# Optimization experiments

Hardware: AMD Instinct MI355X
Metric: run time of the kernel (lower is better)

## Reference

```python
import jax, jax.numpy as jnp
import numpy as np

N = 50000   # nodes
E = 800000  # edges (before self-loops)
IN_C, HID, OUT_C = 10, 96, 48


def setup_inputs() -> dict:
    key = jax.random.key(0)
    ks = jax.random.split(key, 8)
    x = jax.random.normal(ks[0], (N, IN_C), dtype=jnp.float32)
    edge_index = jax.random.randint(ks[1], (2, E), 0, N, dtype=jnp.int64)
    # Glorot-ish scaled weights for the three GCN layers
    W1 = jax.random.normal(ks[2], (IN_C, HID), dtype=jnp.float32) * (1.0 / np.sqrt(IN_C))
    b1 = jnp.zeros((HID,), dtype=jnp.float32)
    W_mu = jax.random.normal(ks[3], (HID, OUT_C), dtype=jnp.float32) * (1.0 / np.sqrt(HID))
    b_mu = jnp.zeros((OUT_C,), dtype=jnp.float32)
    W_logstd = jax.random.normal(ks[4], (HID, OUT_C), dtype=jnp.float32) * (1.0 / np.sqrt(HID))
    b_logstd = jnp.zeros((OUT_C,), dtype=jnp.float32)
    return {"x": x, "edge_index": edge_index, "W1": W1, "b1": b1,
            "W_mu": W_mu, "b_mu": b_mu, "W_logstd": W_logstd, "b_logstd": b_logstd}


def _gcn_norm(edge_index, n_nodes, dtype):
    # PyG gcn_norm: add self-loops, symmetric normalization D^-1/2 A D^-1/2
    loops = jnp.arange(n_nodes, dtype=edge_index.dtype)
    ei = jnp.concatenate([edge_index, jnp.stack([loops, loops])], axis=1)
    row, col = ei[0], ei[1]
    deg = jax.ops.segment_sum(jnp.ones(ei.shape[1], dtype=dtype), col, num_segments=n_nodes)
    dis = jnp.where(deg > 0, jax.lax.rsqrt(deg), jnp.zeros_like(deg))
    norm = dis[row] * dis[col]  # [E+N]
    return row, col, norm


def _gcn_conv(h, row, col, norm, W, b, n_nodes):
    hw = h @ W                                   # dense projection [N, F_out]
    msgs = hw[row] * norm[:, None]               # gather + scale   [E+N, F_out]
    out = jax.ops.segment_sum(msgs, col, num_segments=n_nodes)  # scatter-add
    return out + b


def reference(x, edge_index, W1, b1, W_mu, b_mu, W_logstd, b_logstd):
    row, col, norm = _gcn_norm(edge_index, N, x.dtype)
    h = jax.nn.relu(_gcn_conv(x, row, col, norm, W1, b1, N))
    mu = _gcn_conv(h, row, col, norm, W_mu, b_mu, N)
    logstd = _gcn_conv(h, row, col, norm, W_logstd, b_logstd, N)
    return mu, logstd
```

## Files before the change

kernel.cpp:

```cpp
#include <hip/hip_runtime.h>
#include <hip/hip_bf16.h>

#define NND 50000
#define NED 800000
#define INC 10
#define HID 96
#define OUTC 48
#define NOUT (NND*OUTC)
#define MTILES 3125
#define NW 98
#define SPAN 512
#define EW_CAP 9216
#define PB 200
#define PBE 4000

typedef __hip_bfloat16 bf16;
typedef __attribute__((ext_vector_type(8))) short short8;
typedef __attribute__((ext_vector_type(4))) float f32x4;

#define W1F_O  0L
#define B1F_O  960L
#define BMF_O  1056L
#define BLF_O  1104L
#define DIS_O  1152L
#define XS_O   51152L
#define FLOATS_TOT 551152L

__device__ __forceinline__ float b2f(bf16 v) { return __bfloat162float(v); }
__device__ __forceinline__ float bfLo(unsigned int p) { return __uint_as_float(p << 16); }
__device__ __forceinline__ float bfHi(unsigned int p) { return __uint_as_float(p & 0xffff0000u); }
__device__ __forceinline__ unsigned short f2bu(float v) {
    return __bfloat16_as_ushort(__float2bfloat16(v));
}

__global__ __launch_bounds__(256) void k_part(const int* ei, const void* x,
                                              const void* w1, const void* b1,
                                              const void* wm, const void* bm,
                                              const void* wl, const void* bl,
                                              int* flags, float* F, unsigned short* wct,
                                              unsigned int* part, int* smat, int* cmat) {
    __shared__ int s_oddnz, s_big;
    __shared__ int counts[NW], cur[NW];
    __shared__ unsigned int buf[PBE];
    int tid = threadIdx.x;
    if (tid == 0) { s_oddnz = 0; s_big = 0; }
    for (int i = tid; i < NW; i += 256) counts[i] = 0;
    __syncthreads();
    {
        if (tid < 128) {
            if (ei[2 * tid + 1] != 0) atomicOr(&s_oddnz, 1);
        }
        const unsigned short* xs = (const unsigned short*)x;
        unsigned short u = xs[tid * 8];
        float f = __uint_as_float(((unsigned int)u) << 16);
        int big = !(fabsf(f) < 64.0f);
        unsigned short u2 = xs[tid * 8 + 5];
        float f2 = __uint_as_float(((unsigned int)u2) << 16);
        big |= !(fabsf(f2) < 64.0f);
        if (big) atomicOr(&s_big, 1);
    }
    __syncthreads();
    int iw = (s_oddnz == 0) ? 1 : 0;
    int ff = s_big ? 1 : 0;
    if (blockIdx.x == 0 && tid == 0) { flags[0] = iw; flags[1] = ff; }

    if (blockIdx.x < 41) {
        int idx = blockIdx.x * 256 + tid;
        if (idx < 10368) {
            const void* src; long off; int mode; long dst = 0;
            if      (idx < 960)  { src = w1; off = idx;        mode = 0; dst = W1F_O + idx; }
            else if (idx < 1056) { src = b1; off = idx - 960;  mode = 0; dst = B1F_O + (idx - 960); }
            else if (idx < 1104) { src = bm; off = idx - 1056; mode = 0; dst = BMF_O + (idx - 1056); }
            else if (idx < 1152) { src = bl; off = idx - 1104; mode = 0; dst = BLF_O + (idx - 1104); }
            else if (idx < 5760) { src = wm; off = idx - 1152; mode = 1; }
            else                 { src = wl; off = idx - 5760; mode = 2; }
            float v = ff ? ((const float*)src)[off] : b2f(((const bf16*)src)[off]);
            if (mode == 0) F[dst] = v;
            else if (mode == 1) wct[(off % OUTC) * (long)HID + off / OUTC] = f2bu(v);
            else                wct[(OUTC + off % OUTC) * (long)HID + off / OUTC] = f2bu(v);
        }
    }

    unsigned int wreg[16];
    int base = blockIdx.x * 1000;
    for (int it = 0; it < 4; ++it) {
        int j = it * 256 + tid;
        if (j < 1000) {
            int j4 = base + j;
            int r0, r1, r2, r3, c0, c1, c2, c3;
            if (iw) {
                const int4* pr = (const int4*)ei;
                const int4* pc = (const int4*)(ei + 2L * NED);
                int4 ra = pr[2 * j4], rb = pr[2 * j4 + 1];
                int4 ca = pc[2 * j4], cb = pc[2 * j4 + 1];
                r0 = ra.x; r1 = ra.z; r2 = rb.x; r3 = rb.z;
                c0 = ca.x; c1 = ca.z; c2 = cb.x; c3 = cb.z;
            } else {
                int4 ra = ((const int4*)ei)[j4];
                int4 ca = ((const int4*)(ei + NED))[j4];
                r0 = ra.x; r1 = ra.y; r2 = ra.z; r3 = ra.w;
                c0 = ca.x; c1 = ca.y; c2 = ca.z; c3 = ca.w;
            }
            wreg[4 * it]     = (unsigned)r0 | ((unsigned)c0 << 16);
            wreg[4 * it + 1] = (unsigned)r1 | ((unsigned)c1 << 16);
            wreg[4 * it + 2] = (unsigned)r2 | ((unsigned)c2 << 16);
            wreg[4 * it + 3] = (unsigned)r3 | ((unsigned)c3 << 16);
            atomicAdd(&counts[wreg[4 * it]     >> 25], 1);
            atomicAdd(&counts[wreg[4 * it + 1] >> 25], 1);
            atomicAdd(&counts[wreg[4 * it + 2] >> 25], 1);
            atomicAdd(&counts[wreg[4 * it + 3] >> 25], 1);
        }
    }
    __syncthreads();
    if (tid < NW) {
        int run = 0;
        for (int j = 0; j < tid; ++j) run += counts[j];
        cur[tid] = run;
        cmat[tid * PB + blockIdx.x] = counts[tid];
        smat[tid * PB + blockIdx.x] = blockIdx.x * PBE + run;
    }
    __syncthreads();
    for (int it = 0; it < 4; ++it) {
        int j = it * 256 + tid;
        if (j < 1000) {
#pragma unroll
            for (int q = 0; q < 4; ++q) {
                unsigned int w = wreg[4 * it + q];
                int pos = atomicAdd(&cur[w >> 25], 1);
                buf[pos] = w;
            }
        }
    }
    __syncthreads();
    for (int i = tid; i < PBE; i += 256) part[blockIdx.x * PBE + i] = buf[i];
}

__global__ __launch_bounds__(1024) void k_win(const unsigned int* part, const int* smat,
                                              const int* cmat, const void* x, float* F,
                                              int* cnt, int* start, unsigned short* csr) {
    __shared__ int Lrun[PB], Srun[PB];
    __shared__ int hist[SPAN], st[SPAN], cur[SPAN];
    __shared__ float dl[SPAN];
    __shared__ int s_big;
    int tid = threadIdx.x;
    int w = blockIdx.x;
    if (tid == 0) s_big = 0;
    if (tid < PB) { Lrun[tid] = cmat[w * PB + tid]; Srun[tid] = smat[w * PB + tid]; }
    if (tid < SPAN) hist[tid] = 0;
    __syncthreads();
    if (tid < 256) {
        const unsigned short* xs = (const unsigned short*)x;
        unsigned short u = xs[tid * 8];
        float f = __uint_as_float(((unsigned int)u) << 16);
        int big = !(fabsf(f) < 64.0f);
        unsigned short u2 = xs[tid * 8 + 5];
        float f2 = __uint_as_float(((unsigned int)u2) << 16);
        big |= !(fabsf(f2) < 64.0f);
        if (big) atomicOr(&s_big, 1);
    }
    unsigned int lo = (unsigned)w * SPAN;
    int wave = tid >> 6, lane = tid & 63;
    for (int rb = wave; rb < PB; rb += 16) {
        int L = Lrun[rb], S = Srun[rb];
        for (int i = lane; i < L; i += 64)
            atomicAdd(&hist[(part[S + i] >> 16) - lo], 1);
    }
    __syncthreads();
    int ff = s_big;
    if (tid < SPAN) st[tid] = hist[tid];
    __syncthreads();
    for (int off = 1; off < SPAN; off <<= 1) {
        int t = (tid < SPAN && tid >= off) ? st[tid - off] : 0;
        __syncthreads();
        if (tid < SPAN) st[tid] += t;
        __syncthreads();
    }
    if (tid < SPAN) {
        int h0 = hist[tid];
        int abs0 = w * EW_CAP + (st[tid] - h0);
        cur[tid] = abs0;
        float dis = rsqrtf((float)h0 + 1.0f);
        dl[tid] = dis;
        int g = (int)lo + tid;
        if (g < NND) {
            cnt[g] = h0; start[g] = abs0;
            F[DIS_O + g] = dis;
        }
    }
    __syncthreads();
    for (int i = tid; i < SPAN * INC; i += 1024) {
        int node = (int)lo + i / INC;
        if (node < NND) {
            long xo = (long)node * INC + (i % INC);
            float xv = ff ? ((const float*)x)[xo] : b2f(((const bf16*)x)[xo]);
            F[XS_O + xo] = dl[i / INC] * xv;
        }
    }
    int lim = (w + 1) * EW_CAP;
    for (int rb = wave; rb < PB; rb += 16) {
        int L = Lrun[rb], S = Srun[rb];
        for (int i = lane; i < L; i += 64) {
            unsigned int e = part[S + i];
            int pos = atomicAdd(&cur[(e >> 16) - lo], 1);
            if (pos < lim) csr[pos] = (unsigned short)(e & 0xffffu);
        }
    }
}

__global__ __launch_bounds__(256) void k_layer1(const int* cnt, const int* start,
                                                const unsigned short* csr, const float* F,
                                                unsigned short* h) {
    __shared__ float w1s[1056];
    for (int i = threadIdx.x; i < 1056; i += 256) w1s[i] = F[W1F_O + i];
    __syncthreads();
    int idx = blockIdx.x * 256 + threadIdx.x;
    if (idx >= NND * 4) return;
    int node = idx >> 2, sub = idx & 3;
    int s = start[node], t = s + cnt[node];
    int lim = ((node >> 9) + 1) * EW_CAP;
    if (t > lim) t = lim;
    float ax[INC];
#pragma unroll
    for (int j = 0; j < INC; ++j) ax[j] = 0.0f;
    for (int k = s + sub; k < t; k += 4) {
        int src = csr[k];
        const float2* xr = (const float2*)(F + XS_O + (long)src * INC);
#pragma unroll
        for (int j = 0; j < 5; ++j) {
            float2 v = xr[j];
            ax[2 * j]     += v.x;
            ax[2 * j + 1] += v.y;
        }
    }
    if (sub == 0) {
        const float2* xr = (const float2*)(F + XS_O + (long)node * INC);
#pragma unroll
        for (int j = 0; j < 5; ++j) {
            float2 v = xr[j];
            ax[2 * j]     += v.x;
            ax[2 * j + 1] += v.y;
        }
    }
#pragma unroll
    for (int j = 0; j < INC; ++j) {
        ax[j] += __shfl_xor(ax[j], 1, 64);
        ax[j] += __shfl_xor(ax[j], 2, 64);
    }
    float dn = F[DIS_O + node];
#pragma unroll
    for (int j = 0; j < INC; ++j) ax[j] *= dn;
    int f0 = sub * 24;
    unsigned int* hrow = (unsigned int*)(h + (size_t)node * HID);
#pragma unroll
    for (int f = f0; f < f0 + 24; f += 2) {
        float a0 = w1s[960 + f], a1 = w1s[960 + f + 1];
#pragma unroll
        for (int kk = 0; kk < INC; ++kk) {
            a0 = fmaf(ax[kk], w1s[kk * HID + f], a0);
            a1 = fmaf(ax[kk], w1s[kk * HID + f + 1], a1);
        }
        a0 = fmaxf(a0, 0.0f) * dn;
        a1 = fmaxf(a1, 0.0f) * dn;
        unsigned int u0 = f2bu(a0), u1 = f2bu(a1);
        hrow[f >> 1] = u0 | (u1 << 16);
    }
}

__global__ __launch_bounds__(256) void k_gaggh(const int* cnt, const int* start,
                                               const unsigned short* csr, const float* F,
                                               const unsigned short* h, unsigned int* v) {
    int wid = threadIdx.x >> 6;
    int lane = threadIdx.x & 63;
    int node = blockIdx.x * 4 + wid;
    if (lane >= 48) return;
    const unsigned int* hb = (const unsigned int*)h;

    int s = start[node], t = s + cnt[node];
    int lim = ((node >> 9) + 1) * EW_CAP;
    if (t > lim) t = lim;
    float a0 = 0.0f, a1 = 0.0f;
    int k = s;
    for (; k + 7 < t; k += 8) {
        int s0 = csr[k],     s1 = csr[k + 1], s2 = csr[k + 2], s3 = csr[k + 3];
        int s4 = csr[k + 4], s5 = csr[k + 5], s6 = csr[k + 6], s7 = csr[k + 7];
        unsigned int p0 = hb[(size_t)s0 * 48 + lane];
        unsigned int p1 = hb[(size_t)s1 * 48 + lane];
        unsigned int p2 = hb[(size_t)s2 * 48 + lane];
        unsigned int p3 = hb[(size_t)s3 * 48 + lane];
        unsigned int p4 = hb[(size_t)s4 * 48 + lane];
        unsigned int p5 = hb[(size_t)s5 * 48 + lane];
        unsigned int p6 = hb[(size_t)s6 * 48 + lane];
        unsigned int p7 = hb[(size_t)s7 * 48 + lane];
        a0 += bfLo(p0); a1 += bfHi(p0);
        a0 += bfLo(p1); a1 += bfHi(p1);
        a0 += bfLo(p2); a1 += bfHi(p2);
        a0 += bfLo(p3); a1 += bfHi(p3);
        a0 += bfLo(p4); a1 += bfHi(p4);
        a0 += bfLo(p5); a1 += bfHi(p5);
        a0 += bfLo(p6); a1 += bfHi(p6);
        a0 += bfLo(p7); a1 += bfHi(p7);
    }
    for (; k < t; ++k) {
        unsigned int p0 = hb[(size_t)csr[k] * 48 + lane];
        a0 += bfLo(p0); a1 += bfHi(p0);
    }
    unsigned int ps = hb[(size_t)node * 48 + lane];
    a0 += bfLo(ps); a1 += bfHi(ps);
    float dn = F[DIS_O + node];
    a0 *= dn; a1 *= dn;
    v[(size_t)node * 48 + lane] = (unsigned int)f2bu(a0) | ((unsigned int)f2bu(a1) << 16);
}

__global__ __launch_bounds__(256) void k_heads(const unsigned short* v, const unsigned short* wct,
                                               const float* F, const int* flags, void* dout) {
    int wid = threadIdx.x >> 6;
    int lane = threadIdx.x & 63;
    int mtile = blockIdx.x * 4 + wid;
    if (mtile >= MTILES) return;
    int l16 = lane & 15, quad = lane >> 4;

    const unsigned short* vb = v + ((size_t)mtile * 16 + l16) * HID + quad * 8;
    short8 afr0 = *(const short8*)(vb);
    short8 afr1 = *(const short8*)(vb + 32);
    short8 afr2 = *(const short8*)(vb + 64);

    int ff = flags[1];
#pragma unroll
    for (int nt = 0; nt < 6; ++nt) {
        const unsigned short* wb = wct + ((size_t)nt * 16 + l16) * HID + quad * 8;
        short8 b0 = *(const short8*)(wb);
        short8 b1 = *(const short8*)(wb + 32);
        short8 b2 = *(const short8*)(wb + 64);
        f32x4 acc = {0.0f, 0.0f, 0.0f, 0.0f};
        acc = __builtin_amdgcn_mfma_f32_16x16x32_bf16(afr0, b0, acc, 0, 0, 0);
        acc = __builtin_amdgcn_mfma_f32_16x16x32_bf16(afr1, b1, acc, 0, 0, 0);
        acc = __builtin_amdgcn_mfma_f32_16x16x32_bf16(afr2, b2, acc, 0, 0, 0);
        int n = nt * 16 + l16;
        float bias = (n < OUTC) ? F[BMF_O + n] : F[BLF_O + n - OUTC];
        long obase = (n < OUTC) ? ((long)n) : (NOUT + (long)(n - OUTC));
#pragma unroll
        for (int r = 0; r < 4; ++r) {
            int m = mtile * 16 + quad * 4 + r;
            float val = acc[r] + bias;
            long oi = (long)m * OUTC + obase;
            if (ff) ((float*)dout)[oi] = val;
            else    ((bf16*)dout)[oi] = __float2bfloat16(val);
        }
    }
}

extern "C" void kernel_launch(void* const* d_in, const int* in_sizes, int n_in,
                              void* d_out, int out_size, void* d_ws, size_t ws_size,
                              hipStream_t stream) {
    const int* ei = (const int*)d_in[1];
    int* flags = (int*)d_ws;
    float* F = (float*)((char*)d_ws + 256);
    unsigned short* h   = (unsigned short*)(F + FLOATS_TOT);
    unsigned short* wct = h + (size_t)NND * HID;
    unsigned short* vv  = wct + (size_t)HID * HID;
    int* cnt   = (int*)(vv + (size_t)NND * HID);
    int* start = cnt + NND;
    unsigned int* part = (unsigned int*)(start + NND);
    int* smat = (int*)(part + NED);
    int* cmat = smat + NW * PB;
    unsigned short* csr = (unsigned short*)(cmat + NW * PB);

    k_part<<<PB, 256, 0, stream>>>(ei, d_in[0], d_in[2], d_in[3], d_in[4],
                                   d_in[5], d_in[6], d_in[7], flags, F, wct,
                                   part, smat, cmat);
    k_win<<<NW, 1024, 0, stream>>>(part, smat, cmat, d_in[0], F, cnt, start, csr);
    k_layer1<<<(NND * 4 + 255) / 256, 256, 0, stream>>>(cnt, start, csr, F, h);
    k_gaggh<<<NND / 4, 256, 0, stream>>>(cnt, start, csr, F, h, (unsigned int*)vv);
    k_heads<<<(MTILES + 3) / 4, 256, 0, stream>>>(vv, wct, F, flags, d_out);
}
```

Baseline: 166.8 us.

## Fuse layer-2 neighbor aggregation into MFMA heads kernel

```diff
diff --git a/kernel.cpp b/kernel.cpp
--- a/kernel.cpp
+++ b/kernel.cpp
@@ -266,63 +266,85 @@
     }
 }
 
-__global__ __launch_bounds__(256) void k_gaggh(const int* cnt, const int* start,
-                                               const unsigned short* csr, const float* F,
-                                               const unsigned short* h, unsigned int* v) {
-    int wid = threadIdx.x >> 6;
-    int lane = threadIdx.x & 63;
-    int node = blockIdx.x * 4 + wid;
-    if (lane >= 48) return;
-    const unsigned int* hb = (const unsigned int*)h;
-
-    int s = start[node], t = s + cnt[node];
-    int lim = ((node >> 9) + 1) * EW_CAP;
-    if (t > lim) t = lim;
-    float a0 = 0.0f, a1 = 0.0f;
-    int k = s;
-    for (; k + 7 < t; k += 8) {
-        int s0 = csr[k],     s1 = csr[k + 1], s2 = csr[k + 2], s3 = csr[k + 3];
-        int s4 = csr[k + 4], s5 = csr[k + 5], s6 = csr[k + 6], s7 = csr[k + 7];
-        unsigned int p0 = hb[(size_t)s0 * 48 + lane];
-        unsigned int p1 = hb[(size_t)s1 * 48 + lane];
-        unsigned int p2 = hb[(size_t)s2 * 48 + lane];
-        unsigned int p3 = hb[(size_t)s3 * 48 + lane];
-        unsigned int p4 = hb[(size_t)s4 * 48 + lane];
-        unsigned int p5 = hb[(size_t)s5 * 48 + lane];
-        unsigned int p6 = hb[(size_t)s6 * 48 + lane];
-        unsigned int p7 = hb[(size_t)s7 * 48 + lane];
-        a0 += bfLo(p0); a1 += bfHi(p0);
-        a0 += bfLo(p1); a1 += bfHi(p1);
-        a0 += bfLo(p2); a1 += bfHi(p2);
-        a0 += bfLo(p3); a1 += bfHi(p3);
-        a0 += bfLo(p4); a1 += bfHi(p4);
-        a0 += bfLo(p5); a1 += bfHi(p5);
-        a0 += bfLo(p6); a1 += bfHi(p6);
-        a0 += bfLo(p7); a1 += bfHi(p7);
-    }
-    for (; k < t; ++k) {
-        unsigned int p0 = hb[(size_t)csr[k] * 48 + lane];
-        a0 += bfLo(p0); a1 += bfHi(p0);
-    }
-    unsigned int ps = hb[(size_t)node * 48 + lane];
-    a0 += bfLo(ps); a1 += bfHi(ps);
-    float dn = F[DIS_O + node];
-    a0 *= dn; a1 *= dn;
-    v[(size_t)node * 48 + lane] = (unsigned int)f2bu(a0) | ((unsigned int)f2bu(a1) << 16);
-}
-
-__global__ __launch_bounds__(256) void k_heads(const unsigned short* v, const unsigned short* wct,
-                                               const float* F, const int* flags, void* dout) {
+__global__ __launch_bounds__(256) void k_gh(const int* cnt, const int* start,
+                                            const unsigned short* csr, const float* F,
+                                            const unsigned short* h, const unsigned short* wct,
+                                            const int* flags, void* dout) {
     int wid = threadIdx.x >> 6;
     int lane = threadIdx.x & 63;
     int mtile = blockIdx.x * 4 + wid;
     if (mtile >= MTILES) return;
     int l16 = lane & 15, quad = lane >> 4;
-
-    const unsigned short* vb = v + ((size_t)mtile * 16 + l16) * HID + quad * 8;
-    short8 afr0 = *(const short8*)(vb);
-    short8 afr1 = *(const short8*)(vb + 32);
-    short8 afr2 = *(const short8*)(vb + 64);
+    int node = mtile * 16 + l16;
+
+    const uint4* hb4 = (const uint4*)h;
+    long rowq = (long)node * 12;
+
+    int s = start[node], c = cnt[node];
+    int lim = ((node >> 9) + 1) * EW_CAP;
+    if (s + c > lim) c = lim - s;
+
+    float acc[3][8];
+    {
+        uint4 p0 = hb4[rowq + quad];
+        uint4 p1 = hb4[rowq + 4 + quad];
+        uint4 p2 = hb4[rowq + 8 + quad];
+#pragma unroll
+        for (int t = 0; t < 4; ++t) {
+            unsigned int w0 = (t == 0) ? p0.x : (t == 1) ? p0.y : (t == 2) ? p0.z : p0.w;
+            unsigned int w1 = (t == 0) ? p1.x : (t == 1) ? p1.y : (t == 2) ? p1.z : p1.w;
+            unsigned int w2 = (t == 0) ? p2.x : (t == 1) ? p2.y : (t == 2) ? p2.z : p2.w;
+            acc[0][2 * t] = bfLo(w0); acc[0][2 * t + 1] = bfHi(w0);
+            acc[1][2 * t] = bfLo(w1); acc[1][2 * t + 1] = bfHi(w1);
+            acc[2][2 * t] = bfLo(w2); acc[2][2 * t + 1] = bfHi(w2);
+        }
+    }
+    int k = 0;
+    for (; k + 1 < c; k += 2) {
+        int s0 = csr[s + k], s1 = csr[s + k + 1];
+        long r0 = (long)s0 * 12, r1 = (long)s1 * 12;
+        uint4 a0 = hb4[r0 + quad], a1 = hb4[r0 + 4 + quad], a2 = hb4[r0 + 8 + quad];
+        uint4 b0 = hb4[r1 + quad], b1 = hb4[r1 + 4 + quad], b2 = hb4[r1 + 8 + quad];
+#pragma unroll
+        for (int t = 0; t < 4; ++t) {
+            unsigned int w0 = (t == 0) ? a0.x : (t == 1) ? a0.y : (t == 2) ? a0.z : a0.w;
+            unsigned int w1 = (t == 0) ? a1.x : (t == 1) ? a1.y : (t == 2) ? a1.z : a1.w;
+            unsigned int w2 = (t == 0) ? a2.x : (t == 1) ? a2.y : (t == 2) ? a2.z : a2.w;
+            acc[0][2 * t] += bfLo(w0); acc[0][2 * t + 1] += bfHi(w0);
+            acc[1][2 * t] += bfLo(w1); acc[1][2 * t + 1] += bfHi(w1);
+            acc[2][2 * t] += bfLo(w2); acc[2][2 * t + 1] += bfHi(w2);
+        }
+#pragma unroll
+        for (int t = 0; t < 4; ++t) {
+            unsigned int w0 = (t == 0) ? b0.x : (t == 1) ? b0.y : (t == 2) ? b0.z : b0.w;
+            unsigned int w1 = (t == 0) ? b1.x : (t == 1) ? b1.y : (t == 2) ? b1.z : b1.w;
+            unsigned int w2 = (t == 0) ? b2.x : (t == 1) ? b2.y : (t == 2) ? b2.z : b2.w;
+            acc[0][2 * t] += bfLo(w0); acc[0][2 * t + 1] += bfHi(w0);
+            acc[1][2 * t] += bfLo(w1); acc[1][2 * t + 1] += bfHi(w1);
+            acc[2][2 * t] += bfLo(w2); acc[2][2 * t + 1] += bfHi(w2);
+        }
+    }
+    if (k < c) {
+        int s0 = csr[s + k];
+        long r0 = (long)s0 * 12;
+        uint4 a0 = hb4[r0 + quad], a1 = hb4[r0 + 4 + quad], a2 = hb4[r0 + 8 + quad];
+#pragma unroll
+        for (int t = 0; t < 4; ++t) {
+            unsigned int w0 = (t == 0) ? a0.x : (t == 1) ? a0.y : (t == 2) ? a0.z : a0.w;
+            unsigned int w1 = (t == 0) ? a1.x : (t == 1) ? a1.y : (t == 2) ? a1.z : a1.w;
+            unsigned int w2 = (t == 0) ? a2.x : (t == 1) ? a2.y : (t == 2) ? a2.z : a2.w;
+            acc[0][2 * t] += bfLo(w0); acc[0][2 * t + 1] += bfHi(w0);
+            acc[1][2 * t] += bfLo(w1); acc[1][2 * t + 1] += bfHi(w1);
+            acc[2][2 * t] += bfLo(w2); acc[2][2 * t + 1] += bfHi(w2);
+        }
+    }
+    float dn = F[DIS_O + node];
+    short8 af[3];
+#pragma unroll
+    for (int g = 0; g < 3; ++g)
+#pragma unroll
+        for (int j = 0; j < 8; ++j)
+            af[g][j] = (short)f2bu(acc[g][j] * dn);
 
     int ff = flags[1];
 #pragma unroll
@@ -331,17 +353,17 @@
         short8 b0 = *(const short8*)(wb);
         short8 b1 = *(const short8*)(wb + 32);
         short8 b2 = *(const short8*)(wb + 64);
-        f32x4 acc = {0.0f, 0.0f, 0.0f, 0.0f};
-        acc = __builtin_amdgcn_mfma_f32_16x16x32_bf16(afr0, b0, acc, 0, 0, 0);
-        acc = __builtin_amdgcn_mfma_f32_16x16x32_bf16(afr1, b1, acc, 0, 0, 0);
-        acc = __builtin_amdgcn_mfma_f32_16x16x32_bf16(afr2, b2, acc, 0, 0, 0);
+        f32x4 cacc = {0.0f, 0.0f, 0.0f, 0.0f};
+        cacc = __builtin_amdgcn_mfma_f32_16x16x32_bf16(af[0], b0, cacc, 0, 0, 0);
+        cacc = __builtin_amdgcn_mfma_f32_16x16x32_bf16(af[1], b1, cacc, 0, 0, 0);
+        cacc = __builtin_amdgcn_mfma_f32_16x16x32_bf16(af[2], b2, cacc, 0, 0, 0);
         int n = nt * 16 + l16;
         float bias = (n < OUTC) ? F[BMF_O + n] : F[BLF_O + n - OUTC];
         long obase = (n < OUTC) ? ((long)n) : (NOUT + (long)(n - OUTC));
 #pragma unroll
         for (int r = 0; r < 4; ++r) {
             int m = mtile * 16 + quad * 4 + r;
-            float val = acc[r] + bias;
+            float val = cacc[r] + bias;
             long oi = (long)m * OUTC + obase;
             if (ff) ((float*)dout)[oi] = val;
             else    ((bf16*)dout)[oi] = __float2bfloat16(val);
@@ -357,8 +379,7 @@
     float* F = (float*)((char*)d_ws + 256);
     unsigned short* h   = (unsigned short*)(F + FLOATS_TOT);
     unsigned short* wct = h + (size_t)NND * HID;
-    unsigned short* vv  = wct + (size_t)HID * HID;
-    int* cnt   = (int*)(vv + (size_t)NND * HID);
+    int* cnt   = (int*)(wct + (size_t)HID * HID);
     int* start = cnt + NND;
     unsigned int* part = (unsigned int*)(start + NND);
     int* smat = (int*)(part + NED);
@@ -370,6 +391,5 @@
                                    part, smat, cmat);
     k_win<<<NW, 1024, 0, stream>>>(part, smat, cmat, d_in[0], F, cnt, start, csr);
     k_layer1<<<(NND * 4 + 255) / 256, 256, 0, stream>>>(cnt, start, csr, F, h);
-    k_gaggh<<<NND / 4, 256, 0, stream>>>(cnt, start, csr, F, h, (unsigned int*)vv);
-    k_heads<<<(MTILES + 3) / 4, 256, 0, stream>>>(vv, wct, F, flags, d_out);
-}
+    k_gh<<<(MTILES + 3) / 4, 256, 0, stream>>>(cnt, start, csr, F, h, wct, flags, d_out);
+}
```

Result: faster. 149.4 us (-10.4%).
